# Kernel tuning notes

Measured on AMD Instinct MI355X. Metric: run time of the kernel, lower is better.

## Reference

```python
import jax, jax.numpy as jnp
from jax import lax
import numpy as np

K = 3       # kernel_size
STRIDE = 1
PAD = 1
DIL = 1


def setup_inputs() -> dict:
    key = jax.random.key(0)
    k1, k2, k3, k4 = jax.random.split(key, 4)
    B, C, H, W, Co = 8, 128, 64, 64, 128
    x = jax.random.normal(k1, (B, C, H, W), jnp.float32)
    # offset conv: deformable_groups * 2 * K * K = 18 output channels
    w_off = jax.random.normal(k2, (2 * K * K, C, K, K), jnp.float32) * 0.01
    b_off = jax.random.normal(k3, (2 * K * K,), jnp.float32) * 0.01
    w_dcn = jax.random.normal(k4, (Co, C, K, K), jnp.float32) * (1.0 / np.sqrt(C * K * K))
    return {"x": x, "w_off": w_off, "b_off": b_off, "w_dcn": w_dcn}


def _deform_conv(x, w_off, b_off, w_dcn):
    B, C, H, W = x.shape
    Ho = (H + 2 * PAD - DIL * (K - 1) - 1) // STRIDE + 1
    Wo = (W + 2 * PAD - DIL * (K - 1) - 1) // STRIDE + 1
    KK = K * K

    # --- offset branch: standard conv2d ---
    offset = lax.conv_general_dilated(
        x, w_off, window_strides=(STRIDE, STRIDE),
        padding=[(PAD, PAD), (PAD, PAD)], rhs_dilation=(DIL, DIL),
        dimension_numbers=("NCHW", "OIHW", "NCHW"))
    offset = offset + b_off[None, :, None, None]          # [B, 2*KK, Ho, Wo]
    off = offset.reshape(B, KK, 2, Ho, Wo)
    dy, dx = off[:, :, 0], off[:, :, 1]                   # [B, KK, Ho, Wo]

    # --- sampling coordinates: p0 + p_k + offset ---
    ky, kx = jnp.meshgrid(jnp.arange(K), jnp.arange(K), indexing="ij")
    ky = (ky.reshape(-1) * DIL).astype(x.dtype)           # [KK]
    kx = (kx.reshape(-1) * DIL).astype(x.dtype)
    base_y = (jnp.arange(Ho) * STRIDE - PAD).astype(x.dtype)[None, :, None] + ky[:, None, None]
    base_x = (jnp.arange(Wo) * STRIDE - PAD).astype(x.dtype)[None, None, :] + kx[:, None, None]
    y = base_y[None] + dy                                 # [B, KK, Ho, Wo]
    xc = base_x[None] + dx

    y0 = jnp.floor(y)
    x0 = jnp.floor(xc)
    wy = y - y0                                           # bilinear weights
    wx = xc - x0
    y0i = y0.astype(jnp.int32)
    x0i = x0.astype(jnp.int32)

    def sample_one(xb, y0i, x0i, wy, wx):
        # xb: [C, H, W]; index tensors: [KK, Ho, Wo]
        xf = xb.reshape(C, H * W)

        def corner(iy, ix):
            valid = (iy >= 0) & (iy < H) & (ix >= 0) & (ix < W)   # zero padding
            idx = jnp.clip(iy, 0, H - 1) * W + jnp.clip(ix, 0, W - 1)
            v = jnp.take(xf, idx.reshape(-1), axis=1).reshape(C, KK, Ho, Wo)
            return v * valid[None].astype(xb.dtype)

        v00 = corner(y0i, x0i)
        v01 = corner(y0i, x0i + 1)
        v10 = corner(y0i + 1, x0i)
        v11 = corner(y0i + 1, x0i + 1)
        return (v00 * (1 - wy) * (1 - wx) + v01 * (1 - wy) * wx
                + v10 * wy * (1 - wx) + v11 * wy * wx)      # [C, KK, Ho, Wo]

    sampled = jax.vmap(sample_one)(x, y0i, x0i, wy, wx)      # [B, C, KK, Ho, Wo]

    # --- deformable conv accumulation (groups=1, no bias) ---
    w = w_dcn.reshape(w_dcn.shape[0], C, KK)
    return jnp.einsum("bckhw,ock->bohw", sampled, w)


def reference(x, w_off, b_off, w_dcn):
    return _deform_conv(x, w_off, b_off, w_dcn)
```

## Files before the change

### kernel.cpp

```cpp
#include <hip/hip_runtime.h>

typedef float f32x4 __attribute__((ext_vector_type(4)));
typedef int   i32x4 __attribute__((ext_vector_type(4)));
typedef short b16x8 __attribute__((ext_vector_type(8)));

__device__ __forceinline__ short f2b(float v) {
  union { float f; unsigned u; } x; x.f = v;
  unsigned r = x.u + 0x7FFFu + ((x.u >> 16) & 1u);
  return (short)(r >> 16);
}
__device__ __forceinline__ float b2f(short s) {
  union { unsigned u; float f; } x; x.u = ((unsigned)(unsigned short)s) << 16;
  return x.f;
}

#define WT_ELEMS   (9 * 128 * 128)
#define WOFF_ELEMS (9 * 32 * 128)
#define XT_BYTES   (8u * 4096u * 128u * 2u)

__global__ __launch_bounds__(256) void prep_w(
    const float* __restrict__ w_off, const float* __restrict__ w_dcn,
    short* __restrict__ wT, short* __restrict__ wOffT)
{
  int t = blockIdx.x * 256 + threadIdx.x;
  int stride = gridDim.x * 256;
  for (int i = t; i < WT_ELEMS; i += stride) {
    int j    = i & 7;
    int lane = (i >> 3) & 63;
    int kk   = (i >> 9) & 3;
    int og   = (i >> 11) & 7;
    int k    = i >> 14;
    int o = og * 16 + (lane & 15);
    int c = kk * 32 + (lane >> 4) * 8 + j;
    wT[i] = f2b(w_dcn[o * 1152 + c * 9 + k]);
  }
  for (int i = t; i < WOFF_ELEMS; i += stride) {
    int j    = i & 7;
    int lane = (i >> 3) & 63;
    int kk   = (i >> 9) & 3;
    int fo   = (i >> 11) & 1;
    int k    = i >> 12;
    int o = fo * 16 + (lane & 15);
    int c = kk * 32 + (lane >> 4) * 8 + j;
    wOffT[i] = (o < 18) ? f2b(w_off[o * 1152 + c * 9 + k]) : (short)0;
  }
}

__global__ __launch_bounds__(256) void transp(
    const float* __restrict__ xg, short* __restrict__ xt)
{
  __shared__ float tile[32][65];
  const int bid = blockIdx.x;
  const int b = bid >> 6, y = bid & 63;
  const int t = threadIdx.x;
  const float* src = xg + ((size_t)b << 19) + y * 64;
  short*       dst = xt + ((size_t)b << 19) + (size_t)y * 8192;

  for (int ct = 0; ct < 4; ++ct) {
    __syncthreads();
    int c_l = t >> 3, w0 = (t & 7) * 8;
    const float* p = src + (size_t)(ct * 32 + c_l) * 4096 + w0;
    f32x4 a0 = *(const f32x4*)p;
    f32x4 a1 = *(const f32x4*)(p + 4);
    #pragma unroll
    for (int i = 0; i < 4; ++i) { tile[c_l][w0 + i] = a0[i]; tile[c_l][w0 + 4 + i] = a1[i]; }
    __syncthreads();
    int w = t >> 2, j0 = (t & 3) * 8;
    b16x8 pk;
    #pragma unroll
    for (int j = 0; j < 8; ++j) pk[j] = f2b(tile[j0 + j][w]);
    *(b16x8*)(dst + w * 128 + ct * 32 + j0) = pk;
  }
}

__device__ __forceinline__ void gather8(const short* xb, const i32x4* idxA,
                                        int k, int px_s, int cg, b16x8 (&g)[8]) {
  i32x4 iv = idxA[k * 32 + px_s];
  const short* r0 = xb + (size_t)iv[0] * 128;
  const short* r1 = xb + (size_t)iv[1] * 128;
  const short* r2 = xb + (size_t)iv[2] * 128;
  const short* r3 = xb + (size_t)iv[3] * 128;
  int c0 = cg * 8, c1 = 64 + cg * 8;
  g[0] = *(const b16x8*)(r0 + c0);  g[1] = *(const b16x8*)(r0 + c1);
  g[2] = *(const b16x8*)(r1 + c0);  g[3] = *(const b16x8*)(r1 + c1);
  g[4] = *(const b16x8*)(r2 + c0);  g[5] = *(const b16x8*)(r2 + c1);
  g[6] = *(const b16x8*)(r3 + c0);  g[7] = *(const b16x8*)(r3 + c1);
}

__device__ __forceinline__ void lerp_write(char* sbuf, const f32x4* wtA,
                                           int k, int px_s, int cg, const b16x8 (&g)[8]) {
  f32x4 wv = wtA[k * 32 + px_s];
  #pragma unroll
  for (int it = 0; it < 2; ++it) {
    b16x8 pk;
    #pragma unroll
    for (int j = 0; j < 8; ++j) {
      float v = wv[0] * b2f(g[0 + it][j]) + wv[1] * b2f(g[2 + it][j]) +
                wv[2] * b2f(g[4 + it][j]) + wv[3] * b2f(g[6 + it][j]);
      pk[j] = f2b(v);
    }
    int c0 = it * 64 + cg * 8;
    *(b16x8*)(sbuf + px_s * 256 + ((c0 * 2) ^ ((px_s & 7) << 4))) = pk;
  }
}

__device__ __forceinline__ void mfma_tap(const char* sbuf, const short* wkfrag,
                                         int lane, int l15, int l4,
                                         f32x4& a00, f32x4& a01, f32x4& a10, f32x4& a11) {
  #pragma unroll
  for (int kk = 0; kk < 4; ++kk) {
    int cf = kk * 32 + l4 * 8;
    b16x8 w0 = *(const b16x8*)(wkfrag + ((0 * 4 + kk) << 9) + lane * 8);
    b16x8 w1 = *(const b16x8*)(wkfrag + ((1 * 4 + kk) << 9) + lane * 8);
    b16x8 b0 = *(const b16x8*)(sbuf + l15 * 256        + ((cf * 2) ^ ((l15 & 7) << 4)));
    b16x8 b1 = *(const b16x8*)(sbuf + (16 + l15) * 256 + ((cf * 2) ^ ((l15 & 7) << 4)));
    a00 = __builtin_amdgcn_mfma_f32_16x16x32_bf16(w0, b0, a00, 0, 0, 0);
    a01 = __builtin_amdgcn_mfma_f32_16x16x32_bf16(w0, b1, a01, 0, 0, 0);
    a10 = __builtin_amdgcn_mfma_f32_16x16x32_bf16(w1, b0, a10, 0, 0, 0);
    a11 = __builtin_amdgcn_mfma_f32_16x16x32_bf16(w1, b1, a11, 0, 0, 0);
  }
}

__global__ __launch_bounds__(256, 4) void dcn_mfma(
    const short* __restrict__ xt, const float* __restrict__ b_off,
    const short* __restrict__ wT, const short* __restrict__ wOffT,
    float* __restrict__ out)
{
  __shared__ __align__(16) char  arena[26112];
  __shared__ __align__(16) float offT[32 * 32];

  char*  sW   = arena;
  char*  sS0  = arena;
  char*  sS1  = arena + 8192;
  i32x4* idxA = (i32x4*)(arena + 16384);
  f32x4* wtA  = (f32x4*)(arena + 16384 + 4608);

  const int tid  = threadIdx.x;
  const int lane = tid & 63;
  const int wv_  = tid >> 6;
  const int bid  = blockIdx.x;
  const int swz  = (bid & 7) * 128 + (bid >> 3);
  const int b    = swz >> 7;
  const int ho   = (swz >> 1) & 63;
  const int wo0  = (swz & 1) * 32;

  const int px_s = tid >> 3;
  const int cg   = tid & 7;
  const int l15  = lane & 15;
  const int l4   = lane >> 4;

  const short* xb = xt + ((size_t)b << 19);

  #pragma unroll 1
  for (int i = 0; i < 7; ++i) {
    int s = tid + i * 256;
    if (s < 1632) {
      int p = s >> 4, cc = s & 15;
      int py = p / 34, pxw = p - py * 34;
      int y = ho - 1 + py, xw = wo0 + pxw - 1;
      bool v = ((unsigned)y < 64u) && ((unsigned)xw < 64u);
      b16x8 q = {0,0,0,0,0,0,0,0};
      if (v) q = *(const b16x8*)(xb + ((size_t)(y * 64 + xw) << 7) + cc * 8);
      *(b16x8*)(sW + p * 256 + ((cc * 16) ^ ((p & 7) << 4))) = q;
    }
  }
  __syncthreads();

  f32x4 accP = {0.f, 0.f, 0.f, 0.f};
  const int fo = wv_ >> 1, fp = wv_ & 1;
  {
    const int bpx = fp * 16 + l15;
    #pragma unroll 1
    for (int k = 0; k < 9; ++k) {
      int ky = k / 3, kx = k - ky * 3;
      int p  = ky * 34 + bpx + kx;
      const short* wkf = wOffT + (((k * 2 + fo) * 4) << 9);
      #pragma unroll
      for (int kk = 0; kk < 4; ++kk) {
        int cf = kk * 32 + l4 * 8;
        b16x8 a  = *(const b16x8*)(wkf + (kk << 9) + lane * 8);
        b16x8 bb = *(const b16x8*)(sW + p * 256 + ((cf * 2) ^ ((p & 7) << 4)));
        accP = __builtin_amdgcn_mfma_f32_16x16x32_bf16(a, bb, accP, 0, 0, 0);
      }
    }
  }
  {
    int px = fp * 16 + l15;
    int ob = fo * 16 + l4 * 4;
    #pragma unroll
    for (int r = 0; r < 4; ++r)
      offT[(ob + r) * 32 + px] = accP[r];
  }
  __syncthreads();

  #pragma unroll 1
  for (int i = 0; i < 2; ++i) {
    int item = tid + i * 256;
    if (item < 288) {
      int k = item >> 5, px = item & 31;
      int ky = k / 3, kx = k - ky * 3;
      float dy = offT[(2 * k) * 32 + px]     + b_off[2 * k];
      float dx = offT[(2 * k + 1) * 32 + px] + b_off[2 * k + 1];
      float yy = (float)(ho - 1 + ky) + dy;
      float xx = (float)(wo0 + px - 1 + kx) + dx;
      float y0f = floorf(yy), x0f = floorf(xx);
      float wy = yy - y0f, wx = xx - x0f;
      int y0 = (int)y0f, x0 = (int)x0f;
      int y1 = y0 + 1, x1 = x0 + 1;
      int cy0 = min(max(y0, 0), 63), cx0 = min(max(x0, 0), 63);
      int cy1 = min(max(y1, 0), 63), cx1 = min(max(x1, 0), 63);
      float vy0 = ((unsigned)y0 < 64u) ? 1.f : 0.f;
      float vy1 = ((unsigned)y1 < 64u) ? 1.f : 0.f;
      float vx0 = ((unsigned)x0 < 64u) ? 1.f : 0.f;
      float vx1 = ((unsigned)x1 < 64u) ? 1.f : 0.f;
      i32x4 iv; iv[0] = cy0*64+cx0; iv[1] = cy0*64+cx1; iv[2] = cy1*64+cx0; iv[3] = cy1*64+cx1;
      f32x4 wvv;
      wvv[0] = (1.f - wy) * (1.f - wx) * vy0 * vx0;
      wvv[1] = (1.f - wy) * wx         * vy0 * vx1;
      wvv[2] = wy         * (1.f - wx) * vy1 * vx0;
      wvv[3] = wy         * wx         * vy1 * vx1;
      idxA[item] = iv; wtA[item] = wvv;
    }
  }
  __syncthreads();

  f32x4 acc00 = {0,0,0,0}, acc01 = {0,0,0,0}, acc10 = {0,0,0,0}, acc11 = {0,0,0,0};
  b16x8 g[8];

  #pragma unroll 1
  for (int k = 0; k < 9; ++k) {
    char* sb = (k & 1) ? sS1 : sS0;
    gather8(xb, idxA, k, px_s, cg, g);
    lerp_write(sb, wtA, k, px_s, cg, g);
    __syncthreads();
    const short* wkfrag = wT + (((k * 8 + wv_ * 2) * 4) << 9);
    mfma_tap(sb, wkfrag, lane, l15, l4, acc00, acc01, acc10, acc11);
  }

  {
    size_t base = ((size_t)b * 128) * 4096 + (size_t)ho * 64 + wo0;
    int o0 = wv_ * 32 + l4 * 4;
    #pragma unroll
    for (int r = 0; r < 4; ++r) {
      out[base + (size_t)(o0 + r) * 4096 + l15]           = acc00[r];
      out[base + (size_t)(o0 + r) * 4096 + 16 + l15]      = acc01[r];
      out[base + (size_t)(o0 + 16 + r) * 4096 + l15]      = acc10[r];
      out[base + (size_t)(o0 + 16 + r) * 4096 + 16 + l15] = acc11[r];
    }
  }
}

extern "C" void kernel_launch(void* const* d_in, const int* in_sizes, int n_in,
                              void* d_out, int out_size, void* d_ws, size_t ws_size,
                              hipStream_t stream) {
  const float* x     = (const float*)d_in[0];
  const float* w_off = (const float*)d_in[1];
  const float* b_off = (const float*)d_in[2];
  const float* w_dcn = (const float*)d_in[3];
  float* out = (float*)d_out;

  short* xt    = (short*)d_ws;
  short* wT    = (short*)((char*)d_ws + XT_BYTES);
  short* wOffT = (short*)((char*)d_ws + XT_BYTES + WT_ELEMS * 2);

  hipLaunchKernelGGL(prep_w,   dim3(64),   dim3(256), 0, stream, w_off, w_dcn, wT, wOffT);
  hipLaunchKernelGGL(transp,   dim3(512),  dim3(256), 0, stream, x, xt);
  hipLaunchKernelGGL(dcn_mfma, dim3(1024), dim3(256), 0, stream, xt, b_off, wT, wOffT, out);
}
```

Before: 48.65 us.

## Stage bilinear corner gathers into LDS via direct global-to-LDS loads

Replaces the per-thread register gather of the four bilinear corner rows with wave-cooperative global_load_lds transfers into a new 32KB LDS corner buffer. The lerp then reads the corners back from LDS. The aim is to cut VGPR pressure and use wider, more regular global loads. In exchange, LDS use roughly doubles, the occupancy hint drops from 4 to 2 blocks, and each load is waited on immediately, so no overlap is gained.

```diff
diff --git a/kernel.cpp b/kernel.cpp
--- a/kernel.cpp
+++ b/kernel.cpp
@@ -12,6 +12,12 @@
 __device__ __forceinline__ float b2f(short s) {
   union { unsigned u; float f; } x; x.u = ((unsigned)(unsigned short)s) << 16;
   return x.f;
+}
+
+__device__ __forceinline__ void load_lds16(const void* g, void* l) {
+  __builtin_amdgcn_global_load_lds(
+      (const __attribute__((address_space(1))) unsigned int*)g,
+      (__attribute__((address_space(3))) unsigned int*)l, 16, 0, 0);
 }
 
 #define WT_ELEMS   (9 * 128 * 128)
@@ -73,23 +79,28 @@
   }
 }
 
-__device__ __forceinline__ void gather8(const short* xb, const i32x4* idxA,
-                                        int k, int px_s, int cg, b16x8 (&g)[8]) {
-  i32x4 iv = idxA[k * 32 + px_s];
-  const short* r0 = xb + (size_t)iv[0] * 128;
-  const short* r1 = xb + (size_t)iv[1] * 128;
-  const short* r2 = xb + (size_t)iv[2] * 128;
-  const short* r3 = xb + (size_t)iv[3] * 128;
-  int c0 = cg * 8, c1 = 64 + cg * 8;
-  g[0] = *(const b16x8*)(r0 + c0);  g[1] = *(const b16x8*)(r0 + c1);
-  g[2] = *(const b16x8*)(r1 + c0);  g[3] = *(const b16x8*)(r1 + c1);
-  g[4] = *(const b16x8*)(r2 + c0);  g[5] = *(const b16x8*)(r2 + c1);
-  g[6] = *(const b16x8*)(r3 + c0);  g[7] = *(const b16x8*)(r3 + c1);
-}
-
-__device__ __forceinline__ void lerp_write(char* sbuf, const f32x4* wtA,
-                                           int k, int px_s, int cg, const b16x8 (&g)[8]) {
+__device__ __forceinline__ void stage_corners(const short* xb, const int* idxI,
+                                              char* corners, int k, int wv_, int lane) {
+  const int corner = lane >> 4;
+  const int seg    = lane & 15;
+  #pragma unroll
+  for (int i = 0; i < 8; ++i) {
+    int px = wv_ * 8 + i;
+    int iv = idxI[(k * 32 + px) * 4 + corner];
+    const char* g = (const char*)(xb + (size_t)iv * 128) + seg * 16;
+    load_lds16(g, corners + px * 1024);
+  }
+}
+
+__device__ __forceinline__ void lerp_from_lds(char* sbuf, const char* cbase,
+                                              const f32x4* wtA, int k, int px_s, int cg) {
   f32x4 wv = wtA[k * 32 + px_s];
+  b16x8 g[8];
+  #pragma unroll
+  for (int j = 0; j < 4; ++j) {
+    g[2 * j]     = *(const b16x8*)(cbase + j * 256 + cg * 16);
+    g[2 * j + 1] = *(const b16x8*)(cbase + j * 256 + 128 + cg * 16);
+  }
   #pragma unroll
   for (int it = 0; it < 2; ++it) {
     b16x8 pk;
@@ -121,19 +132,21 @@
   }
 }
 
-__global__ __launch_bounds__(256, 4) void dcn_mfma(
+__global__ __launch_bounds__(256, 2) void dcn_mfma(
     const short* __restrict__ xt, const float* __restrict__ b_off,
     const short* __restrict__ wT, const short* __restrict__ wOffT,
     float* __restrict__ out)
 {
-  __shared__ __align__(16) char  arena[26112];
+  __shared__ __align__(16) char  arena[58368];
   __shared__ __align__(16) float offT[32 * 32];
 
-  char*  sW   = arena;
-  char*  sS0  = arena;
-  char*  sS1  = arena + 8192;
-  i32x4* idxA = (i32x4*)(arena + 16384);
-  f32x4* wtA  = (f32x4*)(arena + 16384 + 4608);
+  char*  sW      = arena;
+  char*  corners = arena;
+  char*  sS0     = arena + 32768;
+  char*  sS1     = arena + 40960;
+  i32x4* idxA    = (i32x4*)(arena + 49152);
+  f32x4* wtA     = (f32x4*)(arena + 53760);
+  const int* idxI = (const int*)(arena + 49152);
 
   const int tid  = threadIdx.x;
   const int lane = tid & 63;
@@ -225,13 +238,14 @@
   __syncthreads();
 
   f32x4 acc00 = {0,0,0,0}, acc01 = {0,0,0,0}, acc10 = {0,0,0,0}, acc11 = {0,0,0,0};
-  b16x8 g[8];
+  const char* cbase = corners + px_s * 1024;
 
   #pragma unroll 1
   for (int k = 0; k < 9; ++k) {
     char* sb = (k & 1) ? sS1 : sS0;
-    gather8(xb, idxA, k, px_s, cg, g);
-    lerp_write(sb, wtA, k, px_s, cg, g);
+    stage_corners(xb, idxI, corners, k, wv_, lane);
+    asm volatile("s_waitcnt vmcnt(0)" ::: "memory");
+    lerp_from_lds(sb, cbase, wtA, k, px_s, cg);
     __syncthreads();
     const short* wkfrag = wT + (((k * 8 + wv_ * 2) * 4) << 9);
     mfma_tap(sb, wkfrag, lane, l15, l4, acc00, acc01, acc10, acc11);
```

After: 70.44 us. +44.8%, slower.

## Stage 5x36 input window in LDS and gather bilinear corners from it

Applied to the files above, without the earlier changes.

Loads a 5-row by 36-column bf16 input window around the output row tile into shared memory, then encodes each bilinear corner as either an LDS window offset or a global-memory fallback index. The per-tap gather reads LDS instead of scattered global rows when the offset stays small, which cuts global gather traffic. In exchange, LDS grows to about 62KB, occupancy drops to 2 blocks/CU, double buffering of the sample tile is replaced by a single buffer with an extra barrier per tap, and the window fill adds upfront load latency.

```diff
diff --git a/kernel.cpp b/kernel.cpp
--- a/kernel.cpp
+++ b/kernel.cpp
@@ -2,6 +2,7 @@
 
 typedef float f32x4 __attribute__((ext_vector_type(4)));
 typedef int   i32x4 __attribute__((ext_vector_type(4)));
+typedef unsigned u32x4 __attribute__((ext_vector_type(4)));
 typedef short b16x8 __attribute__((ext_vector_type(8)));
 
 __device__ __forceinline__ short f2b(float v) {
@@ -17,6 +18,11 @@
 #define WT_ELEMS   (9 * 128 * 128)
 #define WOFF_ELEMS (9 * 32 * 128)
 #define XT_BYTES   (8u * 4096u * 128u * 2u)
+
+#define WIN_OFF   0
+#define SS_OFF    46080
+#define COFS_OFF  54272
+#define WTA_OFF   58880
 
 __global__ __launch_bounds__(256) void prep_w(
     const float* __restrict__ w_off, const float* __restrict__ w_dcn,
@@ -73,23 +79,25 @@
   }
 }
 
-__device__ __forceinline__ void gather8(const short* xb, const i32x4* idxA,
-                                        int k, int px_s, int cg, b16x8 (&g)[8]) {
-  i32x4 iv = idxA[k * 32 + px_s];
-  const short* r0 = xb + (size_t)iv[0] * 128;
-  const short* r1 = xb + (size_t)iv[1] * 128;
-  const short* r2 = xb + (size_t)iv[2] * 128;
-  const short* r3 = xb + (size_t)iv[3] * 128;
-  int c0 = cg * 8, c1 = 64 + cg * 8;
-  g[0] = *(const b16x8*)(r0 + c0);  g[1] = *(const b16x8*)(r0 + c1);
-  g[2] = *(const b16x8*)(r1 + c0);  g[3] = *(const b16x8*)(r1 + c1);
-  g[4] = *(const b16x8*)(r2 + c0);  g[5] = *(const b16x8*)(r2 + c1);
-  g[6] = *(const b16x8*)(r3 + c0);  g[7] = *(const b16x8*)(r3 + c1);
-}
-
-__device__ __forceinline__ void lerp_write(char* sbuf, const f32x4* wtA,
-                                           int k, int px_s, int cg, const b16x8 (&g)[8]) {
+__device__ __forceinline__ void lerp_tap(char* sbuf, const char* win, const short* xb,
+                                         const unsigned* cofsT, const f32x4* wtA,
+                                         int k, int px_s, int cg) {
+  u32x4 co = *(const u32x4*)&cofsT[(k * 32 + px_s) * 4];
   f32x4 wv = wtA[k * 32 + px_s];
+  b16x8 g[8];
+  #pragma unroll
+  for (int c = 0; c < 4; ++c) {
+    unsigned ofs = co[c];
+    if (ofs & 0x80000000u) {
+      const short* gp = xb + (size_t)(ofs & 0x7fffffffu) * 128 + cg * 8;
+      g[2 * c]     = *(const b16x8*)gp;
+      g[2 * c + 1] = *(const b16x8*)(gp + 64);
+    } else {
+      unsigned key = ((ofs >> 8) & 7) << 4;
+      g[2 * c]     = *(const b16x8*)(win + ofs + ((cg * 16) ^ key));
+      g[2 * c + 1] = *(const b16x8*)(win + ofs + 128 + ((cg * 16) ^ key));
+    }
+  }
   #pragma unroll
   for (int it = 0; it < 2; ++it) {
     b16x8 pk;
@@ -121,19 +129,19 @@
   }
 }
 
-__global__ __launch_bounds__(256, 4) void dcn_mfma(
+__global__ __launch_bounds__(256, 2) void dcn_mfma(
     const short* __restrict__ xt, const float* __restrict__ b_off,
     const short* __restrict__ wT, const short* __restrict__ wOffT,
     float* __restrict__ out)
 {
-  __shared__ __align__(16) char  arena[26112];
-  __shared__ __align__(16) float offT[32 * 32];
-
-  char*  sW   = arena;
-  char*  sS0  = arena;
-  char*  sS1  = arena + 8192;
-  i32x4* idxA = (i32x4*)(arena + 16384);
-  f32x4* wtA  = (f32x4*)(arena + 16384 + 4608);
+  __shared__ __align__(16) char arena[63488];
+
+  char*     sW    = arena + WIN_OFF;
+  char*     win   = arena + WIN_OFF;
+  char*     sS    = arena + SS_OFF;
+  float*    offT  = (float*)(arena + SS_OFF);
+  unsigned* cofsT = (unsigned*)(arena + COFS_OFF);
+  f32x4*    wtA   = (f32x4*)(arena + WTA_OFF);
 
   const int tid  = threadIdx.x;
   const int lane = tid & 63;
@@ -184,6 +192,7 @@
       }
     }
   }
+  __syncthreads();
   {
     int px = fp * 16 + l15;
     int ob = fo * 16 + l4 * 4;
@@ -213,28 +222,52 @@
       float vy1 = ((unsigned)y1 < 64u) ? 1.f : 0.f;
       float vx0 = ((unsigned)x0 < 64u) ? 1.f : 0.f;
       float vx1 = ((unsigned)x1 < 64u) ? 1.f : 0.f;
-      i32x4 iv; iv[0] = cy0*64+cx0; iv[1] = cy0*64+cx1; iv[2] = cy1*64+cx0; iv[3] = cy1*64+cx1;
       f32x4 wvv;
       wvv[0] = (1.f - wy) * (1.f - wx) * vy0 * vx0;
       wvv[1] = (1.f - wy) * wx         * vy0 * vx1;
       wvv[2] = wy         * (1.f - wx) * vy1 * vx0;
       wvv[3] = wy         * wx         * vy1 * vx1;
-      idxA[item] = iv; wtA[item] = wvv;
+      int cys[4] = {cy0, cy0, cy1, cy1};
+      int cxs[4] = {cx0, cx1, cx0, cx1};
+      u32x4 enc;
+      #pragma unroll
+      for (int c = 0; c < 4; ++c) {
+        int wr = cys[c] - (ho - 2);
+        int wc = cxs[c] - (wo0 - 2);
+        bool inw = ((unsigned)wr < 5u) && ((unsigned)wc < 36u);
+        enc[c] = inw ? (unsigned)((wr * 36 + wc) * 256)
+                     : (0x80000000u | (unsigned)(cys[c] * 64 + cxs[c]));
+      }
+      *(u32x4*)&cofsT[item * 4] = enc;
+      wtA[item] = wvv;
+    }
+  }
+  __syncthreads();
+
+  #pragma unroll 1
+  for (int i = 0; i < 12; ++i) {
+    int s = tid + i * 256;
+    if (s < 2880) {
+      int seg = s & 15, pos = s >> 4;
+      int r = pos / 36, cc = pos - r * 36;
+      int y = ho - 2 + r, x = wo0 - 2 + cc;
+      bool v = ((unsigned)y < 64u) && ((unsigned)x < 64u);
+      b16x8 q = {0,0,0,0,0,0,0,0};
+      if (v) q = *(const b16x8*)(xb + ((size_t)(y * 64 + x) << 7) + seg * 8);
+      *(b16x8*)(win + pos * 256 + ((seg * 16) ^ ((pos & 7) << 4))) = q;
     }
   }
   __syncthreads();
 
   f32x4 acc00 = {0,0,0,0}, acc01 = {0,0,0,0}, acc10 = {0,0,0,0}, acc11 = {0,0,0,0};
-  b16x8 g[8];
 
   #pragma unroll 1
   for (int k = 0; k < 9; ++k) {
-    char* sb = (k & 1) ? sS1 : sS0;
-    gather8(xb, idxA, k, px_s, cg, g);
-    lerp_write(sb, wtA, k, px_s, cg, g);
+    lerp_tap(sS, win, xb, cofsT, wtA, k, px_s, cg);
     __syncthreads();
     const short* wkfrag = wT + (((k * 8 + wv_ * 2) * 4) << 9);
-    mfma_tap(sb, wkfrag, lane, l15, l4, acc00, acc01, acc10, acc11);
+    mfma_tap(sS, wkfrag, lane, l15, l4, acc00, acc01, acc10, acc11);
+    __syncthreads();
   }
 
   {
```

Result: slower. 61.42 us (+26.2%).
